# Optimization experiments

Hardware: AMD Instinct MI355X
Metric: run time of the kernel (lower is better)

## Reference

```python
import jax, jax.numpy as jnp
import numpy as np

C_LIGHT = 1.0
G_NEWTON = 1.0
COUPLING = 8.0 * np.pi * G_NEWTON / C_LIGHT ** 4  # 8*pi*G/c^4


def _green_kernel():
    # 7x7 Green's-function kernel for Poisson eq: -1/(2*pi*r), center 0
    size, center = 7, 3
    k = np.zeros((1, 1, size, size), np.float32)
    for i in range(size):
        for j in range(size):
            r = np.sqrt((i - center) ** 2 + (j - center) ** 2)
            if r > 0:
                k[0, 0, i, j] = -1.0 / (2.0 * np.pi * r)
    return jnp.asarray(k)


def _gauss_kernel(C):
    # 3x3 separable Gaussian, sigma=1, depthwise (C,1,3,3)
    coords = np.arange(3, dtype=np.float32) - 1.0
    g = np.exp(-coords ** 2 / 2.0)
    g = g / g.sum()
    k = (g[None, :] * g[:, None]).astype(np.float32)
    return jnp.tile(jnp.asarray(k)[None, None], (C, 1, 1, 1))


def _conv(x, k, pad, groups=1):
    return jax.lax.conv_general_dilated(
        x, k, window_strides=(1, 1), padding=[(pad, pad), (pad, pad)],
        dimension_numbers=('NCHW', 'OIHW', 'NCHW'), feature_group_count=groups)


def setup_inputs() -> dict:
    key = jax.random.key(0)
    ks = jax.random.split(key, 20)
    B, H, W = 8, 256, 256
    p = lambda k, shape: (jax.random.normal(k, shape, jnp.float32) * 0.1)
    return {
        'mass': jax.random.uniform(ks[0], (B, H, W, 1), jnp.float32),
        'velocity': jax.random.normal(ks[1], (B, 3), jnp.float32),
        'metric_init': jax.random.normal(ks[2], (B, H, W, 10), jnp.float32),
        # energy net: Linear(4,64) -> GELU -> Linear(64,1) -> Softplus
        'e_w1': p(ks[3], (4, 64)), 'e_b1': jnp.zeros((64,), jnp.float32),
        'e_w2': p(ks[4], (64, 1)), 'e_b2': jnp.zeros((1,), jnp.float32),
        # momentum net: Linear(4,64) -> GELU -> Linear(64,3)
        'm_w1': p(ks[5], (4, 64)), 'm_b1': jnp.zeros((64,), jnp.float32),
        'm_w2': p(ks[6], (64, 3)), 'm_b2': jnp.zeros((3,), jnp.float32),
        # stress net: Linear(4,128) -> GELU -> Linear(128,6)
        's_w1': p(ks[7], (4, 128)), 's_b1': jnp.zeros((128,), jnp.float32),
        's_w2': p(ks[8], (128, 6)), 's_b2': jnp.zeros((6,), jnp.float32),
        'solver_params': jnp.asarray([0.5, 0.3, 0.2], jnp.float32),
    }


def reference(mass, velocity, metric_init,
              e_w1, e_b1, e_w2, e_b2,
              m_w1, m_b1, m_w2, m_b2,
              s_w1, s_b1, s_w2, s_b2,
              solver_params):
    B, H, W, _ = mass.shape
    gelu = lambda x: jax.nn.gelu(x, approximate=False)  # torch exact GELU

    # --- EnergyMomentumTensor: per-pixel MLPs ---
    vel = jnp.broadcast_to(velocity[:, None, None, :], (B, H, W, 3))
    inp = jnp.concatenate([mass, vel], axis=-1).reshape(B * H * W, 4)
    energy = jax.nn.softplus(gelu(inp @ e_w1 + e_b1) @ e_w2 + e_b2)   # [N,1]
    momentum = gelu(inp @ m_w1 + m_b1) @ m_w2 + m_b2                  # [N,3]
    stress = gelu(inp @ s_w1 + s_b1) @ s_w2 + s_b2                    # [N,6]
    T = jnp.concatenate([energy, momentum, stress], axis=-1).reshape(B, H, W, 10)

    # --- EinsteinFieldSolver (linearized) ---
    weights = jax.nn.softmax(solver_params)
    metric = metric_init + weights[0] * (-COUPLING * T)

    mass_n = mass / (mass.max() + 1e-8)
    pot = _conv(mass_n.transpose(0, 3, 1, 2), _green_kernel(), pad=3)[:, 0]  # [B,H,W]
    corr = jnp.zeros((B, H, W, 10), metric.dtype)
    corr = corr.at[..., 4].set(2.0 * G_NEWTON * pot).at[..., 7].set(2.0 * G_NEWTON * pot)
    metric = metric + weights[1] * corr

    # ensure metric validity (signature constraints on diagonal components)
    metric = metric.at[..., 0].set(jnp.minimum(metric[..., 0], -0.1))
    metric = metric.at[..., 4].set(jnp.maximum(metric[..., 4], 0.1))
    metric = metric.at[..., 7].set(jnp.maximum(metric[..., 7], 0.1))
    metric = metric.at[..., 9].set(jnp.maximum(metric[..., 9], 0.1))

    # conditional Gaussian smoothing (weights[2] > 0.1)
    smooth = _conv(metric.transpose(0, 3, 1, 2), _gauss_kernel(10), pad=1,
                   groups=10).transpose(0, 2, 3, 1)
    metric = jnp.where(weights[2] > 0.1, smooth, metric)
    return metric
```

## Files before the change

### kernel.cpp

```cpp
#include <hip/hip_runtime.h>
#include <hip/hip_fp16.h>
#include <math.h>

#define GH 256
#define GW 256
#define NC 10
#define NKNOT 257

__device__ __forceinline__ float gelu_exact(float x) {
    return 0.5f * x * (1.0f + erff(x * 0.70710678118654752f));
}
__device__ __forceinline__ float softplus_f(float x) {
    if (x > 20.f) return x;
    return log1pf(expf(x));
}

__global__ __launch_bounds__(256) void k_pre(
        const float* __restrict__ mass,
        const float* __restrict__ vel,
        const float* __restrict__ e_w1, const float* __restrict__ e_b1,
        const float* __restrict__ e_w2, const float* __restrict__ e_b2,
        const float* __restrict__ m_w1, const float* __restrict__ m_b1,
        const float* __restrict__ m_w2, const float* __restrict__ m_b2,
        const float* __restrict__ s_w1, const float* __restrict__ s_b1,
        const float* __restrict__ s_w2, const float* __restrict__ s_b2,
        float* __restrict__ ws) {
    const int tid = threadIdx.x;
    if (blockIdx.x >= 514) {
        const int pb = blockIdx.x - 514;
        const float4* mass4 = (const float4*)mass;
        int base = pb * 512 + tid;
        float4 a = mass4[base];
        float4 c = mass4[base + 256];
        float v = fmaxf(fmaxf(fmaxf(a.x, a.y), fmaxf(a.z, a.w)),
                        fmaxf(fmaxf(c.x, c.y), fmaxf(c.z, c.w)));
        #pragma unroll
        for (int off = 32; off > 0; off >>= 1)
            v = fmaxf(v, __shfl_xor(v, off, 64));
        __shared__ float sred[4];
        if ((tid & 63) == 0) sred[tid >> 6] = v;
        __syncthreads();
        if (tid == 0)
            ws[pb] = fmaxf(fmaxf(sred[0], sred[1]), fmaxf(sred[2], sred[3]));
        return;
    }
    const int wave = blockIdx.x * 4 + (tid >> 6);
    const int lane = tid & 63;
    const int b = wave / NKNOT, knot = wave % NKNOT;
    const float m = (float)knot * (1.0f / 256.0f);
    const float vx = vel[b * 3 + 0], vy = vel[b * 3 + 1], vz = vel[b * 3 + 2];

    float acc[10];
    {
        float pre = m * e_w1[lane] + vx * e_w1[64 + lane] + vy * e_w1[128 + lane]
                  + vz * e_w1[192 + lane] + e_b1[lane];
        acc[0] = gelu_exact(pre) * e_w2[lane];
    }
    {
        float pre = m * m_w1[lane] + vx * m_w1[64 + lane] + vy * m_w1[128 + lane]
                  + vz * m_w1[192 + lane] + m_b1[lane];
        float h = gelu_exact(pre);
        acc[1] = h * m_w2[lane * 3 + 0];
        acc[2] = h * m_w2[lane * 3 + 1];
        acc[3] = h * m_w2[lane * 3 + 2];
    }
    {
        float pre0 = m * s_w1[lane] + vx * s_w1[128 + lane] + vy * s_w1[256 + lane]
                   + vz * s_w1[384 + lane] + s_b1[lane];
        float pre1 = m * s_w1[64 + lane] + vx * s_w1[192 + lane] + vy * s_w1[320 + lane]
                   + vz * s_w1[448 + lane] + s_b1[64 + lane];
        float h0 = gelu_exact(pre0), h1 = gelu_exact(pre1);
        #pragma unroll
        for (int k = 0; k < 6; k++)
            acc[4 + k] = h0 * s_w2[lane * 6 + k] + h1 * s_w2[(lane + 64) * 6 + k];
    }
    #pragma unroll
    for (int c = 0; c < 10; c++) {
        float v = acc[c];
        #pragma unroll
        for (int off = 32; off > 0; off >>= 1)
            v += __shfl_xor(v, off, 64);
        acc[c] = v;
    }
    if (lane == 0) {
        __half* lut = (__half*)(ws + 1024) + (size_t)(b * NKNOT + knot) * NC;
        lut[0] = __float2half_rn(softplus_f(acc[0] + e_b2[0]));
        lut[1] = __float2half_rn(acc[1] + m_b2[0]);
        lut[2] = __float2half_rn(acc[2] + m_b2[1]);
        lut[3] = __float2half_rn(acc[3] + m_b2[2]);
        #pragma unroll
        for (int k = 0; k < 6; k++)
            lut[4 + k] = __float2half_rn(acc[4 + k] + s_b2[k]);
    }
}

__global__ __launch_bounds__(256, 6) void k_main(const float* __restrict__ mass,
                                                 const float* __restrict__ minit,
                                                 const float* __restrict__ solver,
                                                 const float* __restrict__ ws,
                                                 float* __restrict__ out) {
    const int b = blockIdx.z;
    const int tid = threadIdx.x;
    const int tile_x = blockIdx.x * 16, tile_y = blockIdx.y * 16;

    __shared__ float   s_mass[24][24];
    __shared__ __half2 s_luth[NKNOT * 5];
    __shared__ __align__(16) float2 s_met2[5][18][18];
    __shared__ float   s_wmax[4];

    {
        float v = ws[tid];
        #pragma unroll
        for (int off = 32; off > 0; off >>= 1)
            v = fmaxf(v, __shfl_xor(v, off, 64));
        if ((tid & 63) == 0) s_wmax[tid >> 6] = v;
    }
    {
        const __half2* lutg = (const __half2*)((const __half*)(ws + 1024)
                                               + (size_t)b * NKNOT * NC);
        for (int i = tid; i < NKNOT * 5; i += 256) s_luth[i] = lutg[i];
    }
    {
        const float* mb = minit + (size_t)b * GH * GW * NC;
        for (int i = tid; i < 18 * 90; i += 256) {
            int r = i / 90, c2 = i % 90;
            int px = c2 / 5, cp = c2 % 5;
            int gy = tile_y - 1 + r, gx = tile_x - 1 + px;
            float2 v = make_float2(0.f, 0.f);
            if ((unsigned)gy < GH && (unsigned)gx < GW)
                v = *(const float2*)(mb + ((size_t)gy * GW + gx) * NC + cp * 2);
            s_met2[cp][r][px] = v;
        }
    }
    {
        const float* massb = mass + (size_t)b * GH * GW;
        for (int i = tid; i < 24 * 12; i += 256) {
            int my = i / 12, jx = i % 12;
            int gy = tile_y - 4 + my, gx = tile_x - 4 + 2 * jx;
            float2 v = make_float2(0.f, 0.f);
            if ((unsigned)gy < GH && (unsigned)gx < GW)
                v = *(const float2*)(massb + gy * GW + gx);
            *(float2*)&s_mass[my][2 * jx] = v;
        }
    }
    float p0 = solver[0], p1 = solver[1], p2 = solver[2];
    float pm = fmaxf(p0, fmaxf(p1, p2));
    float e0 = expf(p0 - pm), e1 = expf(p1 - pm), e2 = expf(p2 - pm);
    float inv = 1.f / (e0 + e1 + e2);
    float w0 = e0 * inv, w1 = e1 * inv, w2 = e2 * inv;

    __syncthreads();

    const float gmax = fmaxf(fmaxf(s_wmax[0], s_wmax[1]), fmaxf(s_wmax[2], s_wmax[3]));
    const float k0 = -25.132741228718345f * w0;
    const float potscale = 2.f * w1 / (gmax + 1e-8f);

    for (int idx = tid; idx < 18 * 18; idx += 256) {
        const int ry = idx / 18, rx = idx % 18;
        const int gy = tile_y + ry - 1, gx = tile_x + rx - 1;
        if ((unsigned)gy >= GH || (unsigned)gx >= GW) continue;
        const int cy = ry + 3, cx = rx + 3;
        const float m = s_mass[cy][cx];
        float pot = 0.f;
        #pragma unroll
        for (int dy = 0; dy <= 3; dy++) {
            #pragma unroll
            for (int dx = -3; dx <= 3; dx++) {
                if (dy == 0 && dx <= 0) continue;
                const float wgt = -0.15915494309189535f /
                                  __builtin_sqrtf((float)(dy * dy + dx * dx));
                pot += wgt * (s_mass[cy + dy][cx + dx] + s_mass[cy - dy][cx - dx]);
            }
        }
        const float potterm = potscale * pot;
        float x = m * 256.f;
        int i0 = (int)x;
        i0 = i0 < 255 ? i0 : 255;
        const float f = x - (float)i0;
        const __half2* L0 = &s_luth[i0 * 5];
        #pragma unroll
        for (int cp = 0; cp < 5; cp++) {
            float2 t0 = __half22float2(L0[cp]);
            float2 t1 = __half22float2(L0[cp + 5]);
            float2 r = s_met2[cp][ry][rx];
            r.x = fmaf(k0, fmaf(f, t1.x - t0.x, t0.x), r.x);
            r.y = fmaf(k0, fmaf(f, t1.y - t0.y, t0.y), r.y);
            if (cp == 2) r.x += potterm;
            if (cp == 3) r.y += potterm;
            if (cp == 0) r.x = fminf(r.x, -0.1f);
            if (cp == 2) r.x = fmaxf(r.x, 0.1f);
            if (cp == 3) r.y = fmaxf(r.y, 0.1f);
            if (cp == 4) r.y = fmaxf(r.y, 0.1f);
            s_met2[cp][ry][rx] = r;
        }
    }
    __syncthreads();

    const int oy = tid >> 4, ox = tid & 15;
    const float g0 = 0.274068619f, g1 = 0.451862761f;
    const bool do_smooth = (w2 > 0.1f);
    float2 res[5];
    #pragma unroll
    for (int cp = 0; cp < 5; cp++) {
        if (do_smooth) {
            float2 a0 = s_met2[cp][oy][ox],     a1 = s_met2[cp][oy][ox + 1],     a2 = s_met2[cp][oy][ox + 2];
            float2 b0 = s_met2[cp][oy + 1][ox], b1 = s_met2[cp][oy + 1][ox + 1], b2 = s_met2[cp][oy + 1][ox + 2];
            float2 c0 = s_met2[cp][oy + 2][ox], c1 = s_met2[cp][oy + 2][ox + 1], c2 = s_met2[cp][oy + 2][ox + 2];
            float r0x = fmaf(g0, a0.x + a2.x, g1 * a1.x);
            float r0y = fmaf(g0, a0.y + a2.y, g1 * a1.y);
            float r1x = fmaf(g0, b0.x + b2.x, g1 * b1.x);
            float r1y = fmaf(g0, b0.y + b2.y, g1 * b1.y);
            float r2x = fmaf(g0, c0.x + c2.x, g1 * c1.x);
            float r2y = fmaf(g0, c0.y + c2.y, g1 * c1.y);
            res[cp].x = fmaf(g0, r0x + r2x, g1 * r1x);
            res[cp].y = fmaf(g0, r0y + r2y, g1 * r1y);
        } else {
            res[cp] = s_met2[cp][oy + 1][ox + 1];
        }
    }
    __syncthreads();

    {
        float2* s_out2 = &s_met2[0][0][0];
        #pragma unroll
        for (int cp = 0; cp < 5; cp++)
            s_out2[(oy * 16 + ox) * 5 + cp] = res[cp];
    }
    __syncthreads();

    {
        const float4* s_out4 = (const float4*)&s_met2[0][0][0];
        float* ob = out + ((size_t)(b * GH + tile_y) * GW + tile_x) * NC;
        for (int i = tid; i < 16 * 40; i += 256) {
            int r = i / 40, c4 = i % 40;
            *(float4*)(ob + (size_t)r * GW * NC + c4 * 4) = s_out4[r * 40 + c4];
        }
    }
}

extern "C" void kernel_launch(void* const* d_in, const int* in_sizes, int n_in,
                              void* d_out, int out_size, void* d_ws, size_t ws_size,
                              hipStream_t stream) {
    const float* mass   = (const float*)d_in[0];
    const float* vel    = (const float*)d_in[1];
    const float* minit  = (const float*)d_in[2];
    const float* e_w1   = (const float*)d_in[3];
    const float* e_b1   = (const float*)d_in[4];
    const float* e_w2   = (const float*)d_in[5];
    const float* e_b2   = (const float*)d_in[6];
    const float* m_w1   = (const float*)d_in[7];
    const float* m_b1   = (const float*)d_in[8];
    const float* m_w2   = (const float*)d_in[9];
    const float* m_b2   = (const float*)d_in[10];
    const float* s_w1   = (const float*)d_in[11];
    const float* s_b1   = (const float*)d_in[12];
    const float* s_w2   = (const float*)d_in[13];
    const float* s_b2   = (const float*)d_in[14];
    const float* solver = (const float*)d_in[15];
    float* ws  = (float*)d_ws;
    float* out = (float*)d_out;

    k_pre<<<770, 256, 0, stream>>>(mass, vel, e_w1, e_b1, e_w2, e_b2,
                                   m_w1, m_b1, m_w2, m_b2,
                                   s_w1, s_b1, s_w2, s_b2, ws);
    dim3 grid(16, 16, 8);
    k_main<<<grid, 256, 0, stream>>>(mass, minit, solver, ws, out);
}
```

Baseline: 30.81 us.

## Process two tiles per block, read metric directly, write output directly

Each block now handles two adjacent 16x16 tiles in sequence, so the per-batch LUT load, the global-max reduction and the softmax run once per two tiles, and the grid shrinks to 1024 blocks. The metric_init staging pass into shared memory is dropped: each thread reads its pixel's 10 channels straight from global memory while computing the update. The final output is written directly as float2 per thread instead of being restaged through shared memory for float4 stores. The trade-off is less coalesced global reads and writes (stride of 10 floats per pixel) and half as many blocks to hide latency.

Measured after the change: 28.84 us. 6.4% less time.

```diff
diff --git a/kernel.cpp b/kernel.cpp
--- a/kernel.cpp
+++ b/kernel.cpp
@@ -99,9 +99,12 @@
                                                  const float* __restrict__ solver,
                                                  const float* __restrict__ ws,
                                                  float* __restrict__ out) {
-    const int b = blockIdx.z;
     const int tid = threadIdx.x;
-    const int tile_x = blockIdx.x * 16, tile_y = blockIdx.y * 16;
+    const int bid = blockIdx.x;
+    const int b0 = bid >> 7;
+    const int p  = bid & 127;
+    const int tile_y = (p >> 3) * 16;
+    const int tile_x_base = (p & 7) * 32;
 
     __shared__ float   s_mass[24][24];
     __shared__ __half2 s_luth[NKNOT * 5];
@@ -117,31 +120,8 @@
     }
     {
         const __half2* lutg = (const __half2*)((const __half*)(ws + 1024)
-                                               + (size_t)b * NKNOT * NC);
+                                               + (size_t)b0 * NKNOT * NC);
         for (int i = tid; i < NKNOT * 5; i += 256) s_luth[i] = lutg[i];
-    }
-    {
-        const float* mb = minit + (size_t)b * GH * GW * NC;
-        for (int i = tid; i < 18 * 90; i += 256) {
-            int r = i / 90, c2 = i % 90;
-            int px = c2 / 5, cp = c2 % 5;
-            int gy = tile_y - 1 + r, gx = tile_x - 1 + px;
-            float2 v = make_float2(0.f, 0.f);
-            if ((unsigned)gy < GH && (unsigned)gx < GW)
-                v = *(const float2*)(mb + ((size_t)gy * GW + gx) * NC + cp * 2);
-            s_met2[cp][r][px] = v;
-        }
-    }
-    {
-        const float* massb = mass + (size_t)b * GH * GW;
-        for (int i = tid; i < 24 * 12; i += 256) {
-            int my = i / 12, jx = i % 12;
-            int gy = tile_y - 4 + my, gx = tile_x - 4 + 2 * jx;
-            float2 v = make_float2(0.f, 0.f);
-            if ((unsigned)gy < GH && (unsigned)gx < GW)
-                v = *(const float2*)(massb + gy * GW + gx);
-            *(float2*)&s_mass[my][2 * jx] = v;
-        }
     }
     float p0 = solver[0], p1 = solver[1], p2 = solver[2];
     float pm = fmaxf(p0, fmaxf(p1, p2));
@@ -149,91 +129,108 @@
     float inv = 1.f / (e0 + e1 + e2);
     float w0 = e0 * inv, w1 = e1 * inv, w2 = e2 * inv;
 
-    __syncthreads();
-
-    const float gmax = fmaxf(fmaxf(s_wmax[0], s_wmax[1]), fmaxf(s_wmax[2], s_wmax[3]));
-    const float k0 = -25.132741228718345f * w0;
-    const float potscale = 2.f * w1 / (gmax + 1e-8f);
-
-    for (int idx = tid; idx < 18 * 18; idx += 256) {
-        const int ry = idx / 18, rx = idx % 18;
-        const int gy = tile_y + ry - 1, gx = tile_x + rx - 1;
-        if ((unsigned)gy >= GH || (unsigned)gx >= GW) continue;
-        const int cy = ry + 3, cx = rx + 3;
-        const float m = s_mass[cy][cx];
-        float pot = 0.f;
-        #pragma unroll
-        for (int dy = 0; dy <= 3; dy++) {
-            #pragma unroll
-            for (int dx = -3; dx <= 3; dx++) {
-                if (dy == 0 && dx <= 0) continue;
-                const float wgt = -0.15915494309189535f /
-                                  __builtin_sqrtf((float)(dy * dy + dx * dx));
-                pot += wgt * (s_mass[cy + dy][cx + dx] + s_mass[cy - dy][cx - dx]);
-            }
-        }
-        const float potterm = potscale * pot;
-        float x = m * 256.f;
-        int i0 = (int)x;
-        i0 = i0 < 255 ? i0 : 255;
-        const float f = x - (float)i0;
-        const __half2* L0 = &s_luth[i0 * 5];
-        #pragma unroll
-        for (int cp = 0; cp < 5; cp++) {
-            float2 t0 = __half22float2(L0[cp]);
-            float2 t1 = __half22float2(L0[cp + 5]);
-            float2 r = s_met2[cp][ry][rx];
-            r.x = fmaf(k0, fmaf(f, t1.x - t0.x, t0.x), r.x);
-            r.y = fmaf(k0, fmaf(f, t1.y - t0.y, t0.y), r.y);
-            if (cp == 2) r.x += potterm;
-            if (cp == 3) r.y += potterm;
-            if (cp == 0) r.x = fminf(r.x, -0.1f);
-            if (cp == 2) r.x = fmaxf(r.x, 0.1f);
-            if (cp == 3) r.y = fmaxf(r.y, 0.1f);
-            if (cp == 4) r.y = fmaxf(r.y, 0.1f);
-            s_met2[cp][ry][rx] = r;
-        }
-    }
-    __syncthreads();
-
-    const int oy = tid >> 4, ox = tid & 15;
     const float g0 = 0.274068619f, g1 = 0.451862761f;
     const bool do_smooth = (w2 > 0.1f);
-    float2 res[5];
-    #pragma unroll
-    for (int cp = 0; cp < 5; cp++) {
-        if (do_smooth) {
-            float2 a0 = s_met2[cp][oy][ox],     a1 = s_met2[cp][oy][ox + 1],     a2 = s_met2[cp][oy][ox + 2];
-            float2 b0 = s_met2[cp][oy + 1][ox], b1 = s_met2[cp][oy + 1][ox + 1], b2 = s_met2[cp][oy + 1][ox + 2];
-            float2 c0 = s_met2[cp][oy + 2][ox], c1 = s_met2[cp][oy + 2][ox + 1], c2 = s_met2[cp][oy + 2][ox + 2];
-            float r0x = fmaf(g0, a0.x + a2.x, g1 * a1.x);
-            float r0y = fmaf(g0, a0.y + a2.y, g1 * a1.y);
-            float r1x = fmaf(g0, b0.x + b2.x, g1 * b1.x);
-            float r1y = fmaf(g0, b0.y + b2.y, g1 * b1.y);
-            float r2x = fmaf(g0, c0.x + c2.x, g1 * c1.x);
-            float r2y = fmaf(g0, c0.y + c2.y, g1 * c1.y);
-            res[cp].x = fmaf(g0, r0x + r2x, g1 * r1x);
-            res[cp].y = fmaf(g0, r0y + r2y, g1 * r1y);
-        } else {
-            res[cp] = s_met2[cp][oy + 1][ox + 1];
-        }
-    }
-    __syncthreads();
-
-    {
-        float2* s_out2 = &s_met2[0][0][0];
-        #pragma unroll
-        for (int cp = 0; cp < 5; cp++)
-            s_out2[(oy * 16 + ox) * 5 + cp] = res[cp];
-    }
-    __syncthreads();
-
-    {
-        const float4* s_out4 = (const float4*)&s_met2[0][0][0];
-        float* ob = out + ((size_t)(b * GH + tile_y) * GW + tile_x) * NC;
-        for (int i = tid; i < 16 * 40; i += 256) {
-            int r = i / 40, c4 = i % 40;
-            *(float4*)(ob + (size_t)r * GW * NC + c4 * 4) = s_out4[r * 40 + c4];
+
+    float gmax, k0, potscale;
+
+    #pragma unroll 1
+    for (int sub = 0; sub < 2; sub++) {
+        const int tile_x = tile_x_base + sub * 16;
+
+        if (sub == 1) __syncthreads();
+
+        {
+            const float* massb = mass + (size_t)b0 * GH * GW;
+            for (int i = tid; i < 24 * 12; i += 256) {
+                int my = i / 12, jx = i % 12;
+                int gy = tile_y - 4 + my, gx = tile_x - 4 + 2 * jx;
+                float2 v = make_float2(0.f, 0.f);
+                if ((unsigned)gy < GH && (unsigned)gx < GW)
+                    v = *(const float2*)(massb + gy * GW + gx);
+                *(float2*)&s_mass[my][2 * jx] = v;
+            }
+        }
+        __syncthreads();
+
+        if (sub == 0) {
+            gmax = fmaxf(fmaxf(s_wmax[0], s_wmax[1]), fmaxf(s_wmax[2], s_wmax[3]));
+            k0 = -25.132741228718345f * w0;
+            potscale = 2.f * w1 / (gmax + 1e-8f);
+        }
+
+        for (int idx = tid; idx < 18 * 18; idx += 256) {
+            const int ry = idx / 18, rx = idx % 18;
+            const int gy = tile_y + ry - 1, gx = tile_x + rx - 1;
+            if ((unsigned)gy >= GH || (unsigned)gx >= GW) {
+                #pragma unroll
+                for (int cp = 0; cp < 5; cp++)
+                    s_met2[cp][ry][rx] = make_float2(0.f, 0.f);
+                continue;
+            }
+            const int cy = ry + 3, cx = rx + 3;
+            const float m = s_mass[cy][cx];
+            float pot = 0.f;
+            #pragma unroll
+            for (int dy = 0; dy <= 3; dy++) {
+                #pragma unroll
+                for (int dx = -3; dx <= 3; dx++) {
+                    if (dy == 0 && dx <= 0) continue;
+                    const float wgt = -0.15915494309189535f /
+                                      __builtin_sqrtf((float)(dy * dy + dx * dx));
+                    pot += wgt * (s_mass[cy + dy][cx + dx] + s_mass[cy - dy][cx - dx]);
+                }
+            }
+            const float potterm = potscale * pot;
+            float x = m * 256.f;
+            int i0 = (int)x;
+            i0 = i0 < 255 ? i0 : 255;
+            const float f = x - (float)i0;
+            const __half2* L0 = &s_luth[i0 * 5];
+            const float2* mi2 = (const float2*)(minit + ((size_t)(b0 * GH + gy) * GW + gx) * NC);
+            #pragma unroll
+            for (int cp = 0; cp < 5; cp++) {
+                float2 t0 = __half22float2(L0[cp]);
+                float2 t1 = __half22float2(L0[cp + 5]);
+                float2 mi = mi2[cp];
+                float2 r;
+                r.x = fmaf(k0, fmaf(f, t1.x - t0.x, t0.x), mi.x);
+                r.y = fmaf(k0, fmaf(f, t1.y - t0.y, t0.y), mi.y);
+                if (cp == 2) r.x += potterm;
+                if (cp == 3) r.y += potterm;
+                if (cp == 0) r.x = fminf(r.x, -0.1f);
+                if (cp == 2) r.x = fmaxf(r.x, 0.1f);
+                if (cp == 3) r.y = fmaxf(r.y, 0.1f);
+                if (cp == 4) r.y = fmaxf(r.y, 0.1f);
+                s_met2[cp][ry][rx] = r;
+            }
+        }
+        __syncthreads();
+
+        {
+            const int oy = tid >> 4, ox = tid & 15;
+            const int gy = tile_y + oy, gx = tile_x + ox;
+            float2* outp2 = (float2*)(out + ((size_t)(b0 * GH + gy) * GW + gx) * NC);
+            #pragma unroll
+            for (int cp = 0; cp < 5; cp++) {
+                float2 v;
+                if (do_smooth) {
+                    float2 a0 = s_met2[cp][oy][ox],      a1 = s_met2[cp][oy][ox + 1],      a2 = s_met2[cp][oy][ox + 2];
+                    float2 b0v = s_met2[cp][oy + 1][ox], b1 = s_met2[cp][oy + 1][ox + 1], b2 = s_met2[cp][oy + 1][ox + 2];
+                    float2 c0 = s_met2[cp][oy + 2][ox],  c1 = s_met2[cp][oy + 2][ox + 1], c2 = s_met2[cp][oy + 2][ox + 2];
+                    float r0x = fmaf(g0, a0.x + a2.x, g1 * a1.x);
+                    float r0y = fmaf(g0, a0.y + a2.y, g1 * a1.y);
+                    float r1x = fmaf(g0, b0v.x + b2.x, g1 * b1.x);
+                    float r1y = fmaf(g0, b0v.y + b2.y, g1 * b1.y);
+                    float r2x = fmaf(g0, c0.x + c2.x, g1 * c1.x);
+                    float r2y = fmaf(g0, c0.y + c2.y, g1 * c1.y);
+                    v.x = fmaf(g0, r0x + r2x, g1 * r1x);
+                    v.y = fmaf(g0, r0y + r2y, g1 * r1y);
+                } else {
+                    v = s_met2[cp][oy + 1][ox + 1];
+                }
+                outp2[cp] = v;
+            }
         }
     }
 }
@@ -263,6 +260,5 @@
     k_pre<<<770, 256, 0, stream>>>(mass, vel, e_w1, e_b1, e_w2, e_b2,
                                    m_w1, m_b1, m_w2, m_b2,
                                    s_w1, s_b1, s_w2, s_b2, ws);
-    dim3 grid(16, 16, 8);
-    k_main<<<grid, 256, 0, stream>>>(mass, minit, solver, ws, out);
-}
+    k_main<<<1024, 256, 0, stream>>>(mass, minit, solver, ws, out);
+}
```
